# Kernel optimization log

Hardware: AMD Instinct MI355X
Metric: run time of the kernel (lower is better)

Reference implementation:

```python
import jax, jax.numpy as jnp
import numpy as np

N_MSB = 4
WB = 8       # weight bits
ABNM = 8     # activation bits for non-MVM ops
NL = 0.1     # noise level
B, IN, H = 256, 1024, 1024


def pact_a(x, a):
    # sign(x) * 0.5 * (|x| - ||x|-a| + a)  == sign(x)*min(|x|, a) for a>0
    return jnp.sign(x) * 0.5 * (jnp.abs(x) - jnp.abs(jnp.abs(x) - a) + a)


def _quant_val(x, bits, x_range):
    step = 2.0 ** (bits - 1)
    x01 = jnp.clip(x / x_range, -1.0 + 1.0 / step, 1.0 - 1.0 / step)
    return jnp.round(x01 * step) / step * x_range


def quant_ste(x, bits, x_range):
    # QuantFunc: straight-through estimator (identity grad wrt x, none wrt range)
    return x + jax.lax.stop_gradient(_quant_val(x, bits, x_range) - x)


def bitsplit(x, n_msb):
    # x in [0,1] -> n_msb binary planes stacked on axis 0, plus beta coefficients
    l1 = 2.0 ** n_msb - 1.0
    ys, betas = [], []
    for i in range(n_msb):
        l2 = 2.0 ** (n_msb - (i + 1))
        betas.append(l2 / l1)
        ys.append(jnp.mod(jnp.floor(jnp.round(l1 * x) / l2), 2.0))
    return jnp.stack(ys), jnp.asarray(betas, dtype=x.dtype)


def noisy_qmm(x, w, b, eps_w, eps_b):
    # CustomMM_bmm: quantized weights + gaussian noise in fwd; STE-style bwd.
    w_eff = w + jax.lax.stop_gradient(_quant_val(w, WB, 1.0) - w + eps_w * jnp.max(w) * NL)
    b_eff = b + jax.lax.stop_gradient(_quant_val(b, WB, 1.0) - b + eps_b * jnp.max(b) * NL)
    return jnp.einsum('nbi,nio->nbo', x, w_eff) + b_eff  # [n_msb, B, 4H]


def lstm_cell_q_bs(input, hx, cx, weight_ih, weight_hh, bias_ih, bias_hh,
                   eps_w_ih, eps_w_hh, eps_b_ih, eps_b_hh,
                   a1, a3, a4, a5, a6, a7, a8, a9, a10, a11):
    inp01 = (pact_a(input, a1) + a1) / (a1 * 2.0)            # [B, IN] in [0,1]
    inp_msb, beta = bitsplit(inp01, N_MSB)                   # [n_msb,B,IN], [n_msb]
    o1 = noisy_qmm(inp_msb, weight_ih, bias_ih, eps_w_ih, eps_b_ih)
    o2 = noisy_qmm(inp_msb, weight_hh, bias_hh, eps_w_hh, eps_b_hh)
    out = (o1 > 0.5).astype(inp01.dtype) + (o2 > 0.5).astype(inp01.dtype)
    gates = jnp.einsum('n,nbo->bo', beta, out)               # part1; part2 undefined in source -> 0
    i, j, f, o = jnp.split(gates, 4, axis=1)                 # each [B, H]
    forget_gate_out = quant_ste(pact_a(jax.nn.sigmoid(f), a3), ABNM, a3)
    input_gate_out = quant_ste(pact_a(jax.nn.sigmoid(i), a4), ABNM, a4)
    activation_out = quant_ste(pact_a(jnp.tanh(j), a5), ABNM, a5)
    output_gate_out = quant_ste(pact_a(jax.nn.sigmoid(o), a6), ABNM, a6)
    gated_cell = quant_ste(pact_a(cx * forget_gate_out, a7), ABNM, a7)
    activated_input = quant_ste(pact_a(input_gate_out * activation_out, a8), ABNM, a8)
    new_c = quant_ste(pact_a(gated_cell + activated_input, a9), ABNM, a9)
    activated_cell = quant_ste(pact_a(jnp.tanh(new_c), a10), ABNM, a10)
    new_h = quant_ste(pact_a(activated_cell * output_gate_out, a11), ABNM, a11)
    return new_h, new_c


def setup_inputs() -> dict:
    key = jax.random.key(0)
    ks = jax.random.split(key, 12)
    d = {
        'input': jax.random.normal(ks[0], (B, IN), jnp.float32),
        'hx': jax.random.normal(ks[1], (B, H), jnp.float32),
        'cx': jax.random.normal(ks[2], (B, H), jnp.float32),
        'weight_ih': jax.random.normal(ks[3], (N_MSB, IN, 4 * H), jnp.float32),
        'weight_hh': jax.random.normal(ks[4], (N_MSB, IN, 4 * H), jnp.float32),
        'bias_ih': jax.random.normal(ks[5], (N_MSB, 1, 4 * H), jnp.float32),
        'bias_hh': jax.random.normal(ks[6], (N_MSB, 1, 4 * H), jnp.float32),
        'eps_w_ih': jax.random.normal(ks[7], (N_MSB, IN, 4 * H), jnp.float32),
        'eps_w_hh': jax.random.normal(ks[8], (N_MSB, IN, 4 * H), jnp.float32),
        'eps_b_ih': jax.random.normal(ks[9], (N_MSB, 1, 4 * H), jnp.float32),
        'eps_b_hh': jax.random.normal(ks[10], (N_MSB, 1, 4 * H), jnp.float32),
    }
    a_init = {'a1': 128.0, 'a3': 1.0, 'a4': 1.0, 'a5': 1.0, 'a6': 1.0,
              'a7': 4.0, 'a8': 1.0, 'a9': 4.0, 'a10': 1.0, 'a11': 4.0}
    for name, v in a_init.items():
        d[name] = jnp.array([v], jnp.float32)
    return d


def reference(input, hx, cx, weight_ih, weight_hh, bias_ih, bias_hh,
              eps_w_ih, eps_w_hh, eps_b_ih, eps_b_hh,
              a1, a3, a4, a5, a6, a7, a8, a9, a10, a11):
    return lstm_cell_q_bs(input, hx, cx, weight_ih, weight_hh, bias_ih, bias_hh,
                          eps_w_ih, eps_w_hh, eps_b_ih, eps_b_hh,
                          a1, a3, a4, a5, a6, a7, a8, a9, a10, a11)
```

## Files before the change

kernel.cpp:

```cpp
#include <hip/hip_runtime.h>
#include <hip/hip_bf16.h>
#include <math.h>

typedef int   v4i __attribute__((ext_vector_type(4)));
typedef float v4f __attribute__((ext_vector_type(4)));

#define B_DIM   256
#define IN_DIM  1024
#define H4      4096
#define NPLANE  4
#define WELEM   (NPLANE * IN_DIM * H4)
#define XELEM   (B_DIM * IN_DIM)

#define WS_THRESH_OFF 64
#define WS_X_OFF      (64 + 262144)
#define WS_CMP_OFF    (64 + 262144 + 1048576)

__global__ void k_max(const float* __restrict__ wih, const float* __restrict__ whh,
                      const float* __restrict__ bih, const float* __restrict__ bhh,
                      float* __restrict__ outm) {
  int b = blockIdx.x, t = threadIdx.x;
  const float* src; long n4; int slot; long bb, nb;
  if (b < 512)       { src = wih; n4 = WELEM / 4; slot = 0; bb = b;       nb = 512; }
  else if (b < 1024) { src = whh; n4 = WELEM / 4; slot = 1; bb = b - 512; nb = 512; }
  else if (b == 1024){ src = bih; n4 = 16384 / 4; slot = 2; bb = 0;       nb = 1;   }
  else               { src = bhh; n4 = 16384 / 4; slot = 3; bb = 0;       nb = 1;   }
  const v4f* p = (const v4f*)src;
  float m = -3.4e38f;
  for (long i = bb * 256 + t; i < n4; i += nb * 256) {
    v4f v = p[i];
    m = fmaxf(m, fmaxf(fmaxf(v.x, v.y), fmaxf(v.z, v.w)));
  }
#pragma unroll
  for (int off = 32; off >= 1; off >>= 1) m = fmaxf(m, __shfl_down(m, off, 64));
  __shared__ float sm[4];
  int w = t >> 6, ln = t & 63;
  if (ln == 0) sm[w] = m;
  __syncthreads();
  if (t == 0) {
    m = fmaxf(fmaxf(sm[0], sm[1]), fmaxf(sm[2], sm[3]));
    atomicMax((int*)&outm[slot], __float_as_int(m));
  }
}

__global__ void k_prep(const float* __restrict__ input,
                       const float* __restrict__ bih, const float* __restrict__ bhh,
                       const float* __restrict__ ebih, const float* __restrict__ ebhh,
                       const float* __restrict__ a1p, const float* __restrict__ maxm,
                       double* __restrict__ thresh, signed char* __restrict__ X) {
  int gid = blockIdx.x * 256 + threadIdx.x;
  if (blockIdx.x < 1024) {
    float a1 = a1p[0];
    float x = input[gid];
    float t = fabsf(x), u = fabsf(t - a1);
    float sg = (x > 0.f) ? 0.5f : ((x < 0.f) ? -0.5f : 0.f);
    float p = sg * ((t - u) + a1);
    float inp01 = (p + a1) / (a1 * 2.0f);
    float q = rintf(15.0f * inp01);
    int qi = (int)q;
#pragma unroll
    for (int pl = 0; pl < 4; ++pl)
      X[pl * XELEM + gid] = (signed char)((qi >> (3 - pl)) & 1);
  } else {
    int i2 = gid - 262144;
    int s = i2 >> 14; int r = i2 & 16383;
    const float* bp = s ? bhh : bih;
    const float* ep = s ? ebhh : ebih;
    float mb = maxm[2 + s];
    float bv = bp[r], ev = ep[r];
    float xc = fminf(fmaxf(bv, -0.9921875f), 0.9921875f);
    float qv = rintf(xc * 128.f) * 0.0078125f;
    float noise = (ev * mb) * 0.1f;
    float beff = bv + ((qv - bv) + noise);
    thresh[i2] = 0.5 - (double)beff;
  }
}

__global__ __launch_bounds__(512, 2) void k_gemm(
    const float* __restrict__ Wih, const float* __restrict__ Whh,
    const float* __restrict__ Eih, const float* __restrict__ Ehh,
    const float* __restrict__ maxm, const double* __restrict__ thresh,
    const signed char* __restrict__ X, unsigned char* __restrict__ cmp) {
  const int ntile = blockIdx.x;
  const int sp = blockIdx.y;
  const int s = sp >> 2, plane = sp & 3;
  const float* W = s ? Whh : Wih;
  const float* E = s ? Ehh : Eih;
  const float maxw = maxm[s];

  const int tid = threadIdx.x;
  const int wave = tid >> 6, lane = tid & 63, quad = lane >> 4, l15 = lane & 15;

  __shared__ __align__(16) signed char Blds[2][4][32][80];

  v4i acc[4][2][2];
#pragma unroll
  for (int d = 0; d < 4; ++d)
#pragma unroll
    for (int m = 0; m < 2; ++m)
#pragma unroll
      for (int n = 0; n < 2; ++n) acc[d][m][n] = (v4i){0, 0, 0, 0};

  const size_t wbase = (size_t)plane * IN_DIM * H4 + (size_t)ntile * 32;
  const int kl = tid >> 3;
  const int nc4 = (tid & 7) << 2;

  const signed char* Xp = X + plane * XELEM;
  const int arow0 = wave * 32 + l15;

  auto convert_write = [&](v4f w4, v4f e4, int bf) {
#pragma unroll
    for (int e = 0; e < 4; ++e) {
      float w = w4[e], ev = e4[e];
      float xc = fminf(fmaxf(w, -0.9921875f), 0.9921875f);
      float qv = rintf(xc * 128.f) * 0.0078125f;
      float noise = (ev * maxw) * 0.1f;
      float a = w + ((qv - w) + noise);
      float x0 = a * 8.f;   float f0 = rintf(x0); float r0 = x0 - f0;
      float x1 = r0 * 128.f; float f1 = rintf(x1); float r1 = x1 - f1;
      float x2 = r1 * 128.f; float f2 = rintf(x2); float r2 = x2 - f2;
      float x3 = r2 * 128.f; float f3 = rintf(x3);
      int n = nc4 + e;
      Blds[bf][0][n][kl] = (signed char)(int)f0;
      Blds[bf][1][n][kl] = (signed char)(int)f1;
      Blds[bf][2][n][kl] = (signed char)(int)f2;
      Blds[bf][3][n][kl] = (signed char)(int)f3;
    }
  };

  {
    const float* wp = W + wbase + (size_t)kl * H4 + nc4;
    const float* ep = E + wbase + (size_t)kl * H4 + nc4;
    v4f w4 = *(const v4f*)wp;
    v4f e4 = *(const v4f*)ep;
    convert_write(w4, e4, 0);
  }
  v4i afr[2];
  afr[0] = *(const v4i*)(Xp + (arow0) * IN_DIM + quad * 16);
  afr[1] = *(const v4i*)(Xp + (arow0 + 16) * IN_DIM + quad * 16);
  __syncthreads();

  for (int ch = 0; ch < 16; ++ch) {
    const int buf = ch & 1;
    v4f w4 = {0, 0, 0, 0}, e4 = {0, 0, 0, 0};
    v4i anx[2]; anx[0] = afr[0]; anx[1] = afr[1];
    if (ch < 15) {
      const float* wp = W + wbase + (size_t)((ch + 1) * 64 + kl) * H4 + nc4;
      const float* ep = E + wbase + (size_t)((ch + 1) * 64 + kl) * H4 + nc4;
      w4 = *(const v4f*)wp;
      e4 = *(const v4f*)ep;
      anx[0] = *(const v4i*)(Xp + (arow0) * IN_DIM + (ch + 1) * 64 + quad * 16);
      anx[1] = *(const v4i*)(Xp + (arow0 + 16) * IN_DIM + (ch + 1) * 64 + quad * 16);
    }
#pragma unroll
    for (int d = 0; d < 4; ++d) {
#pragma unroll
      for (int ns = 0; ns < 2; ++ns) {
        v4i bfr = *(const v4i*)&Blds[buf][d][ns * 16 + l15][quad * 16];
        acc[d][0][ns] = __builtin_amdgcn_mfma_i32_16x16x64_i8(afr[0], bfr, acc[d][0][ns], 0, 0, 0);
        acc[d][1][ns] = __builtin_amdgcn_mfma_i32_16x16x64_i8(afr[1], bfr, acc[d][1][ns], 0, 0, 0);
      }
    }
    if (ch < 15) convert_write(w4, e4, buf ^ 1);
    afr[0] = anx[0]; afr[1] = anx[1];
    __syncthreads();
  }

  const double inv = 1.0 / 16777216.0;
  const double* thp = thresh + (size_t)sp * H4;
  unsigned char* cp = cmp + (size_t)sp * B_DIM * H4;
#pragma unroll
  for (int ms = 0; ms < 2; ++ms) {
#pragma unroll
    for (int ns = 0; ns < 2; ++ns) {
      int col = ntile * 32 + ns * 16 + l15;
      double th = thp[col];
#pragma unroll
      for (int r = 0; r < 4; ++r) {
        long long T = ((long long)acc[0][ms][ns][r] << 21) + ((long long)acc[1][ms][ns][r] << 14)
                    + ((long long)acc[2][ms][ns][r] << 7)  +  (long long)acc[3][ms][ns][r];
        int row = wave * 32 + ms * 16 + quad * 4 + r;
        cp[(size_t)row * H4 + col] = ((double)T * inv > th) ? 1 : 0;
      }
    }
  }
}

__device__ __forceinline__ float pact_(float x, float a) {
  float t = fabsf(x), u = fabsf(t - a);
  float sg = (x > 0.f) ? 0.5f : ((x < 0.f) ? -0.5f : 0.f);
  return sg * ((t - u) + a);
}
__device__ __forceinline__ float quant_(float x, float a) {
  float xr = x / a;
  xr = fminf(fmaxf(xr, -0.9921875f), 0.9921875f);
  return rintf(xr * 128.f) * 0.0078125f * a;
}
__device__ __forceinline__ float sigm_(float x) { return 1.0f / (1.0f + expf(-x)); }

__global__ void k_pointwise(const unsigned char* __restrict__ cmp, const float* __restrict__ cx,
                            const float* a3, const float* a4, const float* a5, const float* a6,
                            const float* a7, const float* a8, const float* a9, const float* a10,
                            const float* a11, float* __restrict__ out) {
  int idx = blockIdx.x * 256 + threadIdx.x;
  int b = idx >> 10, h = idx & 1023;
  float g[4];
#pragma unroll
  for (int gi = 0; gi < 4; ++gi) {
    int col = gi * 1024 + h;
    float acc = 0.f;
#pragma unroll
    for (int n = 0; n < 4; ++n) {
      int o = (int)cmp[((size_t)(0 * 4 + n) * B_DIM + b) * H4 + col]
            + (int)cmp[((size_t)(1 * 4 + n) * B_DIM + b) * H4 + col];
      float beta = (float)(8 >> n) / 15.0f;
      acc = acc + beta * (float)o;
    }
    g[gi] = acc;
  }
  float fg = quant_(pact_(sigm_(g[2]), a3[0]), a3[0]);
  float ig = quant_(pact_(sigm_(g[0]), a4[0]), a4[0]);
  float ac = quant_(pact_(tanhf(g[1]), a5[0]), a5[0]);
  float og = quant_(pact_(sigm_(g[3]), a6[0]), a6[0]);
  float cxv = cx[idx];
  float gc = quant_(pact_(cxv * fg, a7[0]), a7[0]);
  float ai = quant_(pact_(ig * ac, a8[0]), a8[0]);
  float nc = quant_(pact_(gc + ai, a9[0]), a9[0]);
  float acl = quant_(pact_(tanhf(nc), a10[0]), a10[0]);
  float nh = quant_(pact_(acl * og, a11[0]), a11[0]);
  out[idx] = nh;
  out[XELEM + idx] = nc;
}

extern "C" void kernel_launch(void* const* d_in, const int* in_sizes, int n_in,
                              void* d_out, int out_size, void* d_ws, size_t ws_size,
                              hipStream_t stream) {
  (void)in_sizes; (void)n_in; (void)out_size; (void)ws_size;
  const float* input = (const float*)d_in[0];
  const float* cx    = (const float*)d_in[2];
  const float* wih   = (const float*)d_in[3];
  const float* whh   = (const float*)d_in[4];
  const float* bih   = (const float*)d_in[5];
  const float* bhh   = (const float*)d_in[6];
  const float* ewih  = (const float*)d_in[7];
  const float* ewhh  = (const float*)d_in[8];
  const float* ebih  = (const float*)d_in[9];
  const float* ebhh  = (const float*)d_in[10];
  const float* a1    = (const float*)d_in[11];
  const float* a3    = (const float*)d_in[12];
  const float* a4    = (const float*)d_in[13];
  const float* a5    = (const float*)d_in[14];
  const float* a6    = (const float*)d_in[15];
  const float* a7    = (const float*)d_in[16];
  const float* a8    = (const float*)d_in[17];
  const float* a9    = (const float*)d_in[18];
  const float* a10   = (const float*)d_in[19];
  const float* a11   = (const float*)d_in[20];
  float* out = (float*)d_out;

  char* ws = (char*)d_ws;
  float*        maxm   = (float*)ws;
  double*       thresh = (double*)(ws + WS_THRESH_OFF);
  signed char*  X      = (signed char*)(ws + WS_X_OFF);
  unsigned char* cmp   = (unsigned char*)(ws + WS_CMP_OFF);

  hipMemsetAsync(ws, 0, 64, stream);
  k_max<<<1026, 256, 0, stream>>>(wih, whh, bih, bhh, maxm);
  k_prep<<<1152, 256, 0, stream>>>(input, bih, bhh, ebih, ebhh, a1, maxm, thresh, X);
  k_gemm<<<dim3(128, 8), 512, 0, stream>>>(wih, whh, ewih, ewhh, maxm, thresh, X, cmp);
  k_pointwise<<<1024, 256, 0, stream>>>(cmp, cx, a3, a4, a5, a6, a7, a8, a9, a10, a11, out);
}
```

Measured before the change: 333.9 us.

## Swizzle int8 weight LDS layout with packed 32-bit writes, fuse bias threshold into GEMM

Each thread now loads 4 consecutive k-rows of one column with scalar loads, packs the four int8 digits per plane into a 32-bit word, and writes it to an XOR-swizzled, unpadded LDS tile. The intent is to replace the many single-byte LDS stores and avoid bank conflicts on the MFMA B-fragment reads. The bias/threshold computation moves from k_prep into the GEMM epilogue, which removes the double-precision threshold buffer. Launch bounds are raised to 4 blocks per CU. The trade-off is less coalesced global loads (scalar, strided by row) and possible register pressure under the tighter launch bound.

```diff
diff --git a/kernel.cpp b/kernel.cpp
--- a/kernel.cpp
+++ b/kernel.cpp
@@ -12,7 +12,6 @@
 #define WELEM   (NPLANE * IN_DIM * H4)
 #define XELEM   (B_DIM * IN_DIM)
 
-#define WS_THRESH_OFF 64
 #define WS_X_OFF      (64 + 262144)
 #define WS_CMP_OFF    (64 + 262144 + 1048576)
 
@@ -43,43 +42,28 @@
   }
 }
 
-__global__ void k_prep(const float* __restrict__ input,
-                       const float* __restrict__ bih, const float* __restrict__ bhh,
-                       const float* __restrict__ ebih, const float* __restrict__ ebhh,
-                       const float* __restrict__ a1p, const float* __restrict__ maxm,
-                       double* __restrict__ thresh, signed char* __restrict__ X) {
+__global__ void k_prep(const float* __restrict__ input, const float* __restrict__ a1p,
+                       signed char* __restrict__ X) {
   int gid = blockIdx.x * 256 + threadIdx.x;
-  if (blockIdx.x < 1024) {
-    float a1 = a1p[0];
-    float x = input[gid];
-    float t = fabsf(x), u = fabsf(t - a1);
-    float sg = (x > 0.f) ? 0.5f : ((x < 0.f) ? -0.5f : 0.f);
-    float p = sg * ((t - u) + a1);
-    float inp01 = (p + a1) / (a1 * 2.0f);
-    float q = rintf(15.0f * inp01);
-    int qi = (int)q;
-#pragma unroll
-    for (int pl = 0; pl < 4; ++pl)
-      X[pl * XELEM + gid] = (signed char)((qi >> (3 - pl)) & 1);
-  } else {
-    int i2 = gid - 262144;
-    int s = i2 >> 14; int r = i2 & 16383;
-    const float* bp = s ? bhh : bih;
-    const float* ep = s ? ebhh : ebih;
-    float mb = maxm[2 + s];
-    float bv = bp[r], ev = ep[r];
-    float xc = fminf(fmaxf(bv, -0.9921875f), 0.9921875f);
-    float qv = rintf(xc * 128.f) * 0.0078125f;
-    float noise = (ev * mb) * 0.1f;
-    float beff = bv + ((qv - bv) + noise);
-    thresh[i2] = 0.5 - (double)beff;
-  }
-}
-
-__global__ __launch_bounds__(512, 2) void k_gemm(
+  float a1 = a1p[0];
+  float x = input[gid];
+  float t = fabsf(x), u = fabsf(t - a1);
+  float sg = (x > 0.f) ? 0.5f : ((x < 0.f) ? -0.5f : 0.f);
+  float p = sg * ((t - u) + a1);
+  float inp01 = (p + a1) / (a1 * 2.0f);
+  float q = rintf(15.0f * inp01);
+  int qi = (int)q;
+#pragma unroll
+  for (int pl = 0; pl < 4; ++pl)
+    X[pl * XELEM + gid] = (signed char)((qi >> (3 - pl)) & 1);
+}
+
+__global__ __launch_bounds__(512, 4) void k_gemm(
     const float* __restrict__ Wih, const float* __restrict__ Whh,
     const float* __restrict__ Eih, const float* __restrict__ Ehh,
-    const float* __restrict__ maxm, const double* __restrict__ thresh,
+    const float* __restrict__ bih, const float* __restrict__ bhh,
+    const float* __restrict__ ebih, const float* __restrict__ ebhh,
+    const float* __restrict__ maxm,
     const signed char* __restrict__ X, unsigned char* __restrict__ cmp) {
   const int ntile = blockIdx.x;
   const int sp = blockIdx.y;
@@ -91,7 +75,12 @@
   const int tid = threadIdx.x;
   const int wave = tid >> 6, lane = tid & 63, quad = lane >> 4, l15 = lane & 15;
 
-  __shared__ __align__(16) signed char Blds[2][4][32][80];
+  __shared__ __align__(16) unsigned char Blds[2 * 4 * 32 * 64];
+
+  const int sn = tid & 31;
+  const int kq = tid >> 5;
+  const int k0 = kq << 2;
+  const int wr_off = sn * 64 + ((((kq >> 2) ^ ((sn >> 1) & 3)) << 4) | ((kq & 3) << 2));
 
   v4i acc[4][2][2];
 #pragma unroll
@@ -101,39 +90,42 @@
 #pragma unroll
       for (int n = 0; n < 2; ++n) acc[d][m][n] = (v4i){0, 0, 0, 0};
 
-  const size_t wbase = (size_t)plane * IN_DIM * H4 + (size_t)ntile * 32;
-  const int kl = tid >> 3;
-  const int nc4 = (tid & 7) << 2;
+  const float* wp = W + (size_t)(plane * IN_DIM + k0) * H4 + (size_t)ntile * 32 + sn;
+  const float* ep = E + (size_t)(plane * IN_DIM + k0) * H4 + (size_t)ntile * 32 + sn;
 
   const signed char* Xp = X + plane * XELEM;
   const int arow0 = wave * 32 + l15;
 
-  auto convert_write = [&](v4f w4, v4f e4, int bf) {
-#pragma unroll
-    for (int e = 0; e < 4; ++e) {
-      float w = w4[e], ev = e4[e];
+  auto digitize_write = [&](const float wv[4], const float evv[4], int bf) {
+    unsigned int pk0 = 0, pk1 = 0, pk2 = 0, pk3 = 0;
+#pragma unroll
+    for (int j = 0; j < 4; ++j) {
+      float w = wv[j], ev = evv[j];
       float xc = fminf(fmaxf(w, -0.9921875f), 0.9921875f);
       float qv = rintf(xc * 128.f) * 0.0078125f;
       float noise = (ev * maxw) * 0.1f;
       float a = w + ((qv - w) + noise);
-      float x0 = a * 8.f;   float f0 = rintf(x0); float r0 = x0 - f0;
+      float x0 = a * 8.f;    float f0 = rintf(x0); float r0 = x0 - f0;
       float x1 = r0 * 128.f; float f1 = rintf(x1); float r1 = x1 - f1;
       float x2 = r1 * 128.f; float f2 = rintf(x2); float r2 = x2 - f2;
       float x3 = r2 * 128.f; float f3 = rintf(x3);
-      int n = nc4 + e;
-      Blds[bf][0][n][kl] = (signed char)(int)f0;
-      Blds[bf][1][n][kl] = (signed char)(int)f1;
-      Blds[bf][2][n][kl] = (signed char)(int)f2;
-      Blds[bf][3][n][kl] = (signed char)(int)f3;
-    }
+      pk0 |= ((unsigned int)((int)f0 & 255)) << (8 * j);
+      pk1 |= ((unsigned int)((int)f1 & 255)) << (8 * j);
+      pk2 |= ((unsigned int)((int)f2 & 255)) << (8 * j);
+      pk3 |= ((unsigned int)((int)f3 & 255)) << (8 * j);
+    }
+    unsigned char* base = Blds + bf * 8192 + wr_off;
+    *(unsigned int*)(base)        = pk0;
+    *(unsigned int*)(base + 2048) = pk1;
+    *(unsigned int*)(base + 4096) = pk2;
+    *(unsigned int*)(base + 6144) = pk3;
   };
 
   {
-    const float* wp = W + wbase + (size_t)kl * H4 + nc4;
-    const float* ep = E + wbase + (size_t)kl * H4 + nc4;
-    v4f w4 = *(const v4f*)wp;
-    v4f e4 = *(const v4f*)ep;
-    convert_write(w4, e4, 0);
+    float w4[4], e4[4];
+#pragma unroll
+    for (int j = 0; j < 4; ++j) { w4[j] = wp[(size_t)j * H4]; e4[j] = ep[(size_t)j * H4]; }
+    digitize_write(w4, e4, 0);
   }
   v4i afr[2];
   afr[0] = *(const v4i*)(Xp + (arow0) * IN_DIM + quad * 16);
@@ -142,39 +134,47 @@
 
   for (int ch = 0; ch < 16; ++ch) {
     const int buf = ch & 1;
-    v4f w4 = {0, 0, 0, 0}, e4 = {0, 0, 0, 0};
+    float nw[4], ne[4];
     v4i anx[2]; anx[0] = afr[0]; anx[1] = afr[1];
     if (ch < 15) {
-      const float* wp = W + wbase + (size_t)((ch + 1) * 64 + kl) * H4 + nc4;
-      const float* ep = E + wbase + (size_t)((ch + 1) * 64 + kl) * H4 + nc4;
-      w4 = *(const v4f*)wp;
-      e4 = *(const v4f*)ep;
+      size_t off = (size_t)(ch + 1) * 64 * H4;
+#pragma unroll
+      for (int j = 0; j < 4; ++j) { nw[j] = wp[off + (size_t)j * H4]; ne[j] = ep[off + (size_t)j * H4]; }
       anx[0] = *(const v4i*)(Xp + (arow0) * IN_DIM + (ch + 1) * 64 + quad * 16);
       anx[1] = *(const v4i*)(Xp + (arow0 + 16) * IN_DIM + (ch + 1) * 64 + quad * 16);
     }
+    const unsigned char* rb = Blds + buf * 8192;
 #pragma unroll
     for (int d = 0; d < 4; ++d) {
 #pragma unroll
       for (int ns = 0; ns < 2; ++ns) {
-        v4i bfr = *(const v4i*)&Blds[buf][d][ns * 16 + l15][quad * 16];
+        const int nr = ns * 16 + l15;
+        v4i bfr = *(const v4i*)(rb + d * 2048 + nr * 64 + ((quad ^ ((nr >> 1) & 3)) << 4));
         acc[d][0][ns] = __builtin_amdgcn_mfma_i32_16x16x64_i8(afr[0], bfr, acc[d][0][ns], 0, 0, 0);
         acc[d][1][ns] = __builtin_amdgcn_mfma_i32_16x16x64_i8(afr[1], bfr, acc[d][1][ns], 0, 0, 0);
       }
     }
-    if (ch < 15) convert_write(w4, e4, buf ^ 1);
+    if (ch < 15) digitize_write(nw, ne, buf ^ 1);
     afr[0] = anx[0]; afr[1] = anx[1];
     __syncthreads();
   }
 
+  const float* bp  = s ? bhh : bih;
+  const float* ebp = s ? ebhh : ebih;
+  const float mb = maxm[2 + s];
   const double inv = 1.0 / 16777216.0;
-  const double* thp = thresh + (size_t)sp * H4;
   unsigned char* cp = cmp + (size_t)sp * B_DIM * H4;
 #pragma unroll
-  for (int ms = 0; ms < 2; ++ms) {
-#pragma unroll
-    for (int ns = 0; ns < 2; ++ns) {
-      int col = ntile * 32 + ns * 16 + l15;
-      double th = thp[col];
+  for (int ns = 0; ns < 2; ++ns) {
+    int col = ntile * 32 + ns * 16 + l15;
+    float bv = bp[plane * H4 + col], ev = ebp[plane * H4 + col];
+    float xc = fminf(fmaxf(bv, -0.9921875f), 0.9921875f);
+    float qv = rintf(xc * 128.f) * 0.0078125f;
+    float noise = (ev * mb) * 0.1f;
+    float beff = bv + ((qv - bv) + noise);
+    double th = 0.5 - (double)beff;
+#pragma unroll
+    for (int ms = 0; ms < 2; ++ms) {
 #pragma unroll
       for (int r = 0; r < 4; ++r) {
         long long T = ((long long)acc[0][ms][ns][r] << 21) + ((long long)acc[1][ms][ns][r] << 14)
@@ -259,14 +259,14 @@
   float* out = (float*)d_out;
 
   char* ws = (char*)d_ws;
-  float*        maxm   = (float*)ws;
-  double*       thresh = (double*)(ws + WS_THRESH_OFF);
-  signed char*  X      = (signed char*)(ws + WS_X_OFF);
-  unsigned char* cmp   = (unsigned char*)(ws + WS_CMP_OFF);
+  float*         maxm = (float*)ws;
+  signed char*   X    = (signed char*)(ws + WS_X_OFF);
+  unsigned char* cmp  = (unsigned char*)(ws + WS_CMP_OFF);
 
   hipMemsetAsync(ws, 0, 64, stream);
   k_max<<<1026, 256, 0, stream>>>(wih, whh, bih, bhh, maxm);
-  k_prep<<<1152, 256, 0, stream>>>(input, bih, bhh, ebih, ebhh, a1, maxm, thresh, X);
-  k_gemm<<<dim3(128, 8), 512, 0, stream>>>(wih, whh, ewih, ewhh, maxm, thresh, X, cmp);
+  k_prep<<<1024, 256, 0, stream>>>(input, a1, X);
+  k_gemm<<<dim3(128, 8), 512, 0, stream>>>(wih, whh, ewih, ewhh, bih, bhh, ebih, ebhh,
+                                           maxm, X, cmp);
   k_pointwise<<<1024, 256, 0, stream>>>(cmp, cx, a3, a4, a5, a6, a7, a8, a9, a10, a11, out);
 }
```

Result: slower. 347.1 us (+4.0%).
